# Performance work log

Hardware: AMD Instinct MI355X
Metric: run time of the kernel (lower is better)

Reference implementation:

```python
import jax, jax.numpy as jnp
import numpy as np

N_USERS = 100000
N_ITEMS = 50000
N_TOTAL = N_USERS + N_ITEMS
IN_DIM = 768
BRANCH = 64
N_EDGES = 2097152
GCN_LAYERS = 3
TEMP = 0.1
BATCH = 4096
NUM_CAND = 128  # neg_per_pos * hard_neg_factor = 16 * 8
NEG = 16


def setup_inputs() -> dict:
    key = jax.random.key(0)
    ks = jax.random.split(key, 12)
    return {
        "raw_item_embs": jax.random.normal(ks[0], (N_ITEMS, IN_DIM), jnp.float32),
        "user_sem_base": jax.random.normal(ks[1], (N_USERS, IN_DIM), jnp.float32),
        "sem_w": jax.random.normal(ks[2], (IN_DIM, BRANCH), jnp.float32) * 0.02,
        "sem_b": jnp.zeros((BRANCH,), jnp.float32),
        "collab_user_w": jax.random.normal(ks[3], (N_USERS, BRANCH), jnp.float32) * 0.1,
        "collab_item_w": jax.random.normal(ks[4], (N_ITEMS, BRANCH), jnp.float32) * 0.1,
        "adj_vals": jax.random.uniform(ks[5], (N_EDGES,), jnp.float32) * 0.1,  # ~normalized adjacency values
        "adj_rows": jax.random.randint(ks[6], (N_EDGES,), 0, N_TOTAL, jnp.int32),
        "adj_cols": jax.random.randint(ks[7], (N_EDGES,), 0, N_TOTAL, jnp.int32),
        "uids": jax.random.randint(ks[8], (BATCH,), 0, N_USERS, jnp.int32),
        "pos_iids": jax.random.randint(ks[9], (BATCH,), 0, N_ITEMS, jnp.int32),
        "cand_ids": jax.random.randint(ks[10], (BATCH, NUM_CAND), 0, N_ITEMS, jnp.int32),
    }


def _normalize(x):
    n = jnp.linalg.norm(x, axis=-1, keepdims=True)
    return x / jnp.maximum(n, 1e-12)


def _forward_embedding(raw_item_embs, user_sem_base, sem_w, sem_b,
                       collab_user_w, collab_item_w, adj_vals, adj_rows, adj_cols):
    # Semantic view (sem_mlp with dropout in eval mode == identity)
    u_sem = _normalize(user_sem_base @ sem_w + sem_b)
    i_sem = _normalize(raw_item_embs @ sem_w + sem_b)
    # Collaborative view: LightGCN propagation over sparse COO adjacency
    ego = jnp.concatenate([collab_user_w, collab_item_w], axis=0)  # [N_TOTAL, BRANCH]
    acc = ego
    for _ in range(GCN_LAYERS):
        msg = adj_vals[:, None] * ego[adj_cols]                     # [E, BRANCH] gather
        ego = jax.ops.segment_sum(msg, adj_rows, num_segments=N_TOTAL)
        acc = acc + ego
    final = acc / (GCN_LAYERS + 1)                                  # mean over stacked layers
    u_collab = _normalize(final[:N_USERS])
    i_collab = _normalize(final[N_USERS:])
    # Norm-Concat-Norm fusion
    u_all = _normalize(jnp.concatenate([u_collab, u_sem], axis=1))  # [N_USERS, 2*BRANCH]
    i_all = _normalize(jnp.concatenate([i_collab, i_sem], axis=1))  # [N_ITEMS, 2*BRANCH]
    return u_all, i_all


def reference(raw_item_embs, user_sem_base, sem_w, sem_b, collab_user_w,
              collab_item_w, adj_vals, adj_rows, adj_cols, uids, pos_iids, cand_ids):
    all_u, all_i = _forward_embedding(raw_item_embs, user_sem_base, sem_w, sem_b,
                                      collab_user_w, collab_item_w,
                                      adj_vals, adj_rows, adj_cols)
    batch_u = all_u[uids]          # [B, D]
    batch_pos = all_i[pos_iids]    # [B, D]
    # Dynamic hard negative mining (no_grad block in torch)
    pos_mask = cand_ids == pos_iids[:, None]
    cands = jnp.where(pos_mask, (cand_ids + 1) % N_ITEMS, cand_ids)  # [B, C]
    cand_embs = jax.lax.stop_gradient(all_i)[cands]                  # [B, C, D]
    cand_scores = jnp.einsum('bcd,bd->bc', cand_embs, jax.lax.stop_gradient(batch_u))
    _, top_idx = jax.lax.top_k(cand_scores, NEG)                     # [B, NEG]
    hard_neg_ids = jnp.take_along_axis(cands, top_idx, axis=1)       # [B, NEG]
    batch_neg = all_i[hard_neg_ids]                                  # [B, NEG, D]
    pos_logit = jnp.sum(batch_u * batch_pos, axis=-1, keepdims=True) / TEMP  # [B, 1]
    neg_logit = jnp.einsum('bnd,bd->bn', batch_neg, batch_u) / TEMP          # [B, NEG]
    logits = jnp.concatenate([pos_logit, neg_logit], axis=1)                 # [B, 1+NEG]
    # cross-entropy with labels = 0
    loss = -jnp.mean(jax.nn.log_softmax(logits, axis=-1)[:, 0])
    return loss
```

## Files before the change

kernel.cpp:

```cpp
#include <hip/hip_runtime.h>
#include <hip/hip_bf16.h>

#define N_USERS 100000
#define N_ITEMS 50000
#define N_TOTAL 150000
#define IN_DIM 768
#define BRANCH 64
#define N_EDGES 2097152
#define BATCH 4096
#define NUM_CAND 128
#define NEG 16
#define TEMP 0.1f
#define D2 128

#define NB 586
#define BH_BLOCKS 1024

typedef short short8 __attribute__((ext_vector_type(8)));
typedef float f32x4 __attribute__((ext_vector_type(4)));

__device__ __forceinline__ unsigned short f2bf(float f) {
    unsigned int u = __builtin_bit_cast(unsigned int, f);
    u += 0x7fffu + ((u >> 16) & 1u);
    return (unsigned short)(u >> 16);
}


__global__ __launch_bounds__(256) void bucket_hist(const int* __restrict__ rows,
                                                   int* __restrict__ bcnt) {
    __shared__ int h[NB];
    int t = threadIdx.x;
    long base = (long)blockIdx.x * 2048;
    for (int b = t; b < NB; b += 256) h[b] = 0;
    __syncthreads();
    #pragma unroll
    for (int k = 0; k < 8; ++k)
        atomicAdd(&h[rows[base + k * 256 + t] >> 8], 1);
    __syncthreads();
    for (int b = t; b < NB; b += 256) {
        int c = h[b];
        if (c) atomicAdd(&bcnt[b], c);
    }
}

__global__ __launch_bounds__(256) void bucket_scan(const int* __restrict__ bcnt,
                                                   int* __restrict__ boff,
                                                   int* __restrict__ bcur,
                                                   int* __restrict__ offs) {
    int t = threadIdx.x;
    int fi = t * 4;
    int a0 = (fi + 0 < NB) ? bcnt[fi + 0] : 0;
    int a1 = (fi + 1 < NB) ? bcnt[fi + 1] : 0;
    int a2 = (fi + 2 < NB) ? bcnt[fi + 2] : 0;
    int a3 = (fi + 3 < NB) ? bcnt[fi + 3] : 0;
    int sm = a0 + a1 + a2 + a3;
    int x = sm;
    int lane = t & 63, wid = t >> 6;
    #pragma unroll
    for (int off = 1; off < 64; off <<= 1) {
        int y = __shfl_up(x, off);
        if (lane >= off) x += y;
    }
    __shared__ int wsum[4], woff[4];
    if (lane == 63) wsum[wid] = x;
    __syncthreads();
    if (t == 0) {
        int r = 0;
        for (int i = 0; i < 4; ++i) { woff[i] = r; r += wsum[i]; }
    }
    __syncthreads();
    int excl = (x - sm) + woff[wid];
    int p[5];
    p[0] = excl;
    p[1] = p[0] + a0;
    p[2] = p[1] + a1;
    p[3] = p[2] + a2;
    p[4] = p[3] + a3;
    #pragma unroll
    for (int k = 0; k < 4; ++k) {
        if (fi + k < NB) { boff[fi + k] = p[k]; bcur[fi + k] = p[k]; }
    }
    if (fi <= NB && NB < fi + 4) {
        boff[NB] = p[NB - fi];
        offs[N_TOTAL] = p[NB - fi];
    }
}

__global__ __launch_bounds__(256) void bucket_scatter(const int* __restrict__ rows,
                                                      const int* __restrict__ cols,
                                                      const float* __restrict__ vals,
                                                      int* __restrict__ bcur,
                                                      int2* __restrict__ bedges) {
    __shared__ int lcnt[NB];
    __shared__ int lbase[NB];
    int t = threadIdx.x;
    long base = (long)blockIdx.x * 2048;
    for (int b = t; b < NB; b += 256) lcnt[b] = 0;
    __syncthreads();
    int r[8], pk[8], vb[8];
    #pragma unroll
    for (int k = 0; k < 8; ++k) {
        long i = base + k * 256 + t;
        int rr = rows[i];
        r[k]  = rr;
        pk[k] = ((rr & 255) << 18) | cols[i];
        vb[k] = __float_as_int(vals[i]);
        atomicAdd(&lcnt[rr >> 8], 1);
    }
    __syncthreads();
    for (int b = t; b < NB; b += 256) {
        int c = lcnt[b];
        if (c) lbase[b] = atomicAdd(&bcur[b], c);
    }
    __syncthreads();
    #pragma unroll
    for (int k = 0; k < 8; ++k) {
        int p = atomicAdd(&lbase[r[k] >> 8], 1);
        bedges[p] = make_int2(pk[k], vb[k]);
    }
}

__global__ __launch_bounds__(256) void fine_scatter(const int* __restrict__ boff,
                                                    const int2* __restrict__ bedges,
                                                    int* __restrict__ offs,
                                                    int2* __restrict__ edges) {
    __shared__ int hist_[256];
    __shared__ int curp[256];
    __shared__ int wsum[4], woff[4];
    int t = threadIdx.x, lane = t & 63, wid = t >> 6;
    int b = blockIdx.x;
    int s = boff[b], e = boff[b + 1];
    hist_[t] = 0;
    __syncthreads();
    for (int i = s + t; i < e; i += 256)
        atomicAdd(&hist_[((unsigned)bedges[i].x) >> 18], 1);
    __syncthreads();
    int orig = hist_[t];
    int x = orig;
    #pragma unroll
    for (int off = 1; off < 64; off <<= 1) {
        int y = __shfl_up(x, off);
        if (lane >= off) x += y;
    }
    if (lane == 63) wsum[wid] = x;
    __syncthreads();
    if (t == 0) {
        int r = 0;
        for (int i = 0; i < 4; ++i) { woff[i] = r; r += wsum[i]; }
    }
    __syncthreads();
    int excl = x - orig + woff[wid];
    int row = b * 256 + t;
    if (row < N_TOTAL) offs[row] = s + excl;
    curp[t] = s + excl;
    __syncthreads();
    for (int i = s + t; i < e; i += 256) {
        int2 rec = bedges[i];
        int rl = ((unsigned)rec.x) >> 18;
        int p = atomicAdd(&curp[rl], 1);
        edges[p] = make_int2(rec.x & 0x3FFFF, rec.y);
    }
}


__global__ __launch_bounds__(256) void init_ego_kernel(const float* __restrict__ uw,
                                                       const float* __restrict__ iw,
                                                       float* __restrict__ ego,
                                                       float* __restrict__ acc) {
    long i = (long)blockIdx.x * blockDim.x + threadIdx.x;
    const long n4 = (long)N_TOTAL * BRANCH / 4;
    if (i >= n4) return;
    long fi = i * 4;
    const long usz = (long)N_USERS * BRANCH;
    float4 v;
    if (fi < usz) v = *(const float4*)(uw + fi);
    else          v = *(const float4*)(iw + (fi - usz));
    *(float4*)(ego + fi) = v;
    *(float4*)(acc + fi) = v;
}

__global__ __launch_bounds__(256) void spmv_kernel(const int* __restrict__ offs,
                                                   const int2* __restrict__ edges,
                                                   const float* __restrict__ ego_in,
                                                   float* __restrict__ ego_out,
                                                   float* __restrict__ acc,
                                                   int write_ego) {
    int wave = (blockIdx.x * 256 + threadIdx.x) >> 6;
    int lane = threadIdx.x & 63;
    int sub  = lane >> 4;
    int l16  = lane & 15;
    int row  = wave * 4 + sub;
    if (row >= N_TOTAL) return;

    int s = offs[row], e = offs[row + 1];
    f32x4 sum = {0.f, 0.f, 0.f, 0.f};

    int i  = s;
    int e4 = s + ((e - s) & ~3);
    for (; i < e4; i += 4) {
        int2 p0 = edges[i];
        int2 p1 = edges[i + 1];
        int2 p2 = edges[i + 2];
        int2 p3 = edges[i + 3];
        f32x4 g0 = *(const f32x4*)(ego_in + (long)p0.x * BRANCH + l16 * 4);
        f32x4 g1 = *(const f32x4*)(ego_in + (long)p1.x * BRANCH + l16 * 4);
        f32x4 g2 = *(const f32x4*)(ego_in + (long)p2.x * BRANCH + l16 * 4);
        f32x4 g3 = *(const f32x4*)(ego_in + (long)p3.x * BRANCH + l16 * 4);
        sum += g0 * __int_as_float(p0.y);
        sum += g1 * __int_as_float(p1.y);
        sum += g2 * __int_as_float(p2.y);
        sum += g3 * __int_as_float(p3.y);
    }
    for (; i < e; ++i) {
        int2 p = edges[i];
        f32x4 g = *(const f32x4*)(ego_in + (long)p.x * BRANCH + l16 * 4);
        sum += g * __int_as_float(p.y);
    }

    long o = (long)row * BRANCH + l16 * 4;
    if (write_ego) *(f32x4*)(ego_out + o) = sum;
    f32x4 a = *(const f32x4*)(acc + o);
    a += sum;
    *(f32x4*)(acc + o) = a;
}


__global__ __launch_bounds__(256) void wt_prep(const float* __restrict__ W,
                                               unsigned short* __restrict__ gWt) {
    int idx = blockIdx.x * 256 + threadIdx.x;
    if (idx >= 64 * IN_DIM) return;
    int n = idx / IN_DIM, k = idx % IN_DIM;
    gWt[idx] = f2bf(W[(long)k * 64 + n]);
}

#define GROWS 128
#define GK 32
#define LSTR 40

__global__ __launch_bounds__(256) void sem_gemm_mfma(const float* __restrict__ user_base,
                                                     const float* __restrict__ item_base,
                                                     const unsigned short* __restrict__ gWt,
                                                     const float* __restrict__ bias,
                                                     float* __restrict__ all_emb) {
    __shared__ unsigned short Asl[GROWS * LSTR];
    __shared__ unsigned short Wsl[64 * LSTR];

    const int tid  = threadIdx.x;
    const int row0 = blockIdx.x * GROWS;
    const int wv   = tid >> 6;
    const int lane = tid & 63;
    const int l15  = lane & 15;
    const int quad = lane >> 4;

    const int s_r = tid >> 3;
    const int s_c = (tid & 7) * 4;

    f32x4 acc[2][4];
    #pragma unroll
    for (int r = 0; r < 2; ++r)
        #pragma unroll
        for (int c = 0; c < 4; ++c)
            acc[r][c] = (f32x4){0.f, 0.f, 0.f, 0.f};

    const int wt_n  = tid >> 2;
    const int wt_c8 = (tid & 3) * 8;

    for (int kt = 0; kt < IN_DIM; kt += GK) {
        #pragma unroll
        for (int i = 0; i < 4; ++i) {
            int r = s_r + i * 32;
            int gr = row0 + r;
            if (gr >= N_TOTAL) gr = 0;
            const float* src = (gr < N_USERS) ? (user_base + (long)gr * IN_DIM)
                                              : (item_base + (long)(gr - N_USERS) * IN_DIM);
            float4 v = *(const float4*)(src + kt + s_c);
            unsigned short* d = &Asl[r * LSTR + s_c];
            d[0] = f2bf(v.x); d[1] = f2bf(v.y); d[2] = f2bf(v.z); d[3] = f2bf(v.w);
        }
        {
            uint4 v = *(const uint4*)(gWt + (long)wt_n * IN_DIM + kt + wt_c8);
            *(uint4*)(&Wsl[wt_n * LSTR + wt_c8]) = v;
        }
        __syncthreads();

        const int arow = wv * 32 + l15;
        short8 a0 = *(const short8*)(&Asl[arow * LSTR + quad * 8]);
        short8 a1 = *(const short8*)(&Asl[(arow + 16) * LSTR + quad * 8]);
        short8 b[4];
        #pragma unroll
        for (int c = 0; c < 4; ++c)
            b[c] = *(const short8*)(&Wsl[(c * 16 + l15) * LSTR + quad * 8]);
        #pragma unroll
        for (int c = 0; c < 4; ++c) {
            acc[0][c] = __builtin_amdgcn_mfma_f32_16x16x32_bf16(a0, b[c], acc[0][c], 0, 0, 0);
            acc[1][c] = __builtin_amdgcn_mfma_f32_16x16x32_bf16(a1, b[c], acc[1][c], 0, 0, 0);
        }
        __syncthreads();
    }

    #pragma unroll
    for (int r = 0; r < 2; ++r) {
        #pragma unroll
        for (int c = 0; c < 4; ++c) {
            int col = c * 16 + l15;
            float bv = bias[col];
            #pragma unroll
            for (int i = 0; i < 4; ++i) {
                int gr = row0 + wv * 32 + r * 16 + quad * 4 + i;
                if (gr < N_TOTAL)
                    all_emb[(long)gr * D2 + BRANCH + col] = acc[r][c][i] + bv;
            }
        }
    }
}


__global__ __launch_bounds__(256) void fuse_kernel(const float* __restrict__ acc,
                                                   float* __restrict__ all_emb) {
    int wave = (blockIdx.x * 256 + threadIdx.x) >> 6;
    int lane = threadIdx.x & 63;
    if (wave >= N_TOTAL) return;

    float c = acc[(long)wave * BRANCH + lane] * 0.25f;
    float cs = c * c;
    #pragma unroll
    for (int off = 1; off < 64; off <<= 1) cs += __shfl_xor(cs, off);
    float cn = c / fmaxf(sqrtf(cs), 1e-12f);

    float s = all_emb[(long)wave * D2 + BRANCH + lane];
    float ss = s * s;
    #pragma unroll
    for (int off = 1; off < 64; off <<= 1) ss += __shfl_xor(ss, off);
    float sn = s / fmaxf(sqrtf(ss), 1e-12f);

    float tt = cn * cn + sn * sn;
    #pragma unroll
    for (int off = 1; off < 64; off <<= 1) tt += __shfl_xor(tt, off);
    float inv = 1.0f / fmaxf(sqrtf(tt), 1e-12f);

    all_emb[(long)wave * D2 + lane]          = cn * inv;
    all_emb[(long)wave * D2 + BRANCH + lane] = sn * inv;
}


__global__ __launch_bounds__(128) void loss_kernel(const float* __restrict__ all_emb,
                                                   const int* __restrict__ uids,
                                                   const int* __restrict__ pos_iids,
                                                   const int* __restrict__ cand_ids,
                                                   float* __restrict__ out) {
    __shared__ __align__(16) float uL[128];
    __shared__ float sc[128];
    __shared__ float redv[128];
    __shared__ int   ridx[128];
    __shared__ float topvals[NEG];

    int b = blockIdx.x;
    int t = threadIdx.x;
    int uid = uids[b];
    int pid = pos_iids[b];
    const float* ib = all_emb + (long)N_USERS * D2;

    uL[t] = all_emb[(long)uid * D2 + t];
    __syncthreads();

    redv[t] = uL[t] * ib[(long)pid * D2 + t];
    __syncthreads();
    for (int st = 64; st > 0; st >>= 1) {
        if (t < st) redv[t] += redv[t + st];
        __syncthreads();
    }
    float pos_dot = redv[0];

    int cand = cand_ids[(long)b * NUM_CAND + t];
    if (cand == pid) cand = (cand + 1) % N_ITEMS;
    const float4* cr4 = (const float4*)(ib + (long)cand * D2);
    const float4* u4  = (const float4*)uL;
    float s = 0.f;
    #pragma unroll 8
    for (int k = 0; k < 32; ++k) {
        float4 a = cr4[k];
        float4 u = u4[k];
        s += a.x * u.x + a.y * u.y + a.z * u.z + a.w * u.w;
    }
    sc[t] = s;
    __syncthreads();

    for (int it = 0; it < NEG; ++it) {
        redv[t] = sc[t];
        ridx[t] = t;
        __syncthreads();
        for (int st = 64; st > 0; st >>= 1) {
            if (t < st) {
                if (redv[t + st] > redv[t]) { redv[t] = redv[t + st]; ridx[t] = ridx[t + st]; }
            }
            __syncthreads();
        }
        if (t == 0) {
            topvals[it] = redv[0];
            sc[ridx[0]] = -3.0e38f;
        }
        __syncthreads();
    }

    if (t == 0) {
        float pl = pos_dot / TEMP;
        float m = pl;
        #pragma unroll
        for (int i = 0; i < NEG; ++i) m = fmaxf(m, topvals[i] / TEMP);
        float se = __expf(pl - m);
        #pragma unroll
        for (int i = 0; i < NEG; ++i) se += __expf(topvals[i] / TEMP - m);
        float lse = m + __logf(se);
        atomicAdd(out, (lse - pl) * (1.0f / BATCH));
    }
}


extern "C" void kernel_launch(void* const* d_in, const int* in_sizes, int n_in,
                              void* d_out, int out_size, void* d_ws, size_t ws_size,
                              hipStream_t stream) {
    const float* raw_item_embs = (const float*)d_in[0];
    const float* user_sem_base = (const float*)d_in[1];
    const float* sem_w         = (const float*)d_in[2];
    const float* sem_b         = (const float*)d_in[3];
    const float* collab_user_w = (const float*)d_in[4];
    const float* collab_item_w = (const float*)d_in[5];
    const float* adj_vals      = (const float*)d_in[6];
    const int*   adj_rows      = (const int*)d_in[7];
    const int*   adj_cols      = (const int*)d_in[8];
    const int*   uids          = (const int*)d_in[9];
    const int*   pos_iids      = (const int*)d_in[10];
    const int*   cand_ids      = (const int*)d_in[11];
    float* out = (float*)d_out;

    float* all_emb = (float*)d_ws;
    float* acc     = all_emb + (long)N_TOTAL * D2;
    float* egoA    = acc  + (long)N_TOTAL * BRANCH;
    float* egoB    = egoA + (long)N_TOTAL * BRANCH;
    int*   offs    = (int*)(egoB + (long)N_TOTAL * BRANCH);
    int*   bmeta   = offs + (N_TOTAL + 4);
    int*   bcnt    = bmeta;
    int*   boff    = bmeta + 1024;
    int*   bcur    = bmeta + 2048;
    int2*  edges   = (int2*)(bmeta + N_TOTAL);
    int*   bsums   = (int*)(edges + N_EDGES);
    unsigned short* gWt = (unsigned short*)(bsums + 256);
    int2*  bedges  = (int2*)egoB;

    hipMemsetAsync(bcnt, 0, 1024 * sizeof(int), stream);
    hipMemsetAsync(out, 0, sizeof(float), stream);

    bucket_hist   <<<BH_BLOCKS, 256, 0, stream>>>(adj_rows, bcnt);
    bucket_scan   <<<1, 256, 0, stream>>>(bcnt, boff, bcur, offs);
    bucket_scatter<<<BH_BLOCKS, 256, 0, stream>>>(adj_rows, adj_cols, adj_vals, bcur, bedges);
    fine_scatter  <<<NB, 256, 0, stream>>>(boff, bedges, offs, edges);

    init_ego_kernel<<<(N_TOTAL * BRANCH / 4 + 255) / 256, 256, 0, stream>>>(
        collab_user_w, collab_item_w, egoA, acc);
    const int spmv_blocks = (N_TOTAL + 15) / 16;
    spmv_kernel<<<spmv_blocks, 256, 0, stream>>>(offs, edges, egoA, egoB, acc, 1);
    spmv_kernel<<<spmv_blocks, 256, 0, stream>>>(offs, edges, egoB, egoA, acc, 1);
    spmv_kernel<<<spmv_blocks, 256, 0, stream>>>(offs, edges, egoA, egoB, acc, 0);

    wt_prep<<<(64 * IN_DIM + 255) / 256, 256, 0, stream>>>(sem_w, gWt);
    sem_gemm_mfma<<<(N_TOTAL + GROWS - 1) / GROWS, 256, 0, stream>>>(
        user_sem_base, raw_item_embs, gWt, sem_b, all_emb);

    fuse_kernel<<<37500, 256, 0, stream>>>(acc, all_emb);

    loss_kernel<<<BATCH, 128, 0, stream>>>(all_emb, uids, pos_iids, cand_ids, out);
}
```

Before: 1.050 ms.

## Compute user semantics only for batch users and drop histogram pass

Runs the semantic GEMM and the fusion step only for the BATCH users actually referenced by uids, not all 100k users, which removes most of the 768-wide user read. Keeps all four GCN layer outputs in separate buffers so the SpMV no longer does an accumulator read-modify-write. Merges the bucket histogram into the scatter by using fixed-capacity buckets (CAP), which saves one pass over the edge rows. It also swaps the shared-memory top-k loop for wave-shuffle reductions. The fixed bucket capacity assumes no 256-row bucket receives more than CAP edges, which holds only for roughly uniform row distributions.

```diff
diff --git a/kernel.cpp b/kernel.cpp
--- a/kernel.cpp
+++ b/kernel.cpp
@@ -14,6 +14,7 @@
 #define D2 128
 
 #define NB 586
+#define CAP 5120
 #define BH_BLOCKS 1024
 
 typedef short short8 __attribute__((ext_vector_type(8)));
@@ -26,26 +27,43 @@
 }
 
 
-__global__ __launch_bounds__(256) void bucket_hist(const int* __restrict__ rows,
-                                                   int* __restrict__ bcnt) {
-    __shared__ int h[NB];
+__global__ __launch_bounds__(256) void bucket_scatter(const int* __restrict__ rows,
+                                                      const int* __restrict__ cols,
+                                                      const float* __restrict__ vals,
+                                                      int* __restrict__ bcnt,
+                                                      int2* __restrict__ bedges) {
+    __shared__ int lcnt[NB];
+    __shared__ int lbase[NB];
     int t = threadIdx.x;
     long base = (long)blockIdx.x * 2048;
-    for (int b = t; b < NB; b += 256) h[b] = 0;
-    __syncthreads();
-    #pragma unroll
-    for (int k = 0; k < 8; ++k)
-        atomicAdd(&h[rows[base + k * 256 + t] >> 8], 1);
+    for (int b = t; b < NB; b += 256) lcnt[b] = 0;
+    __syncthreads();
+    int r[8], pk[8], vb[8];
+    #pragma unroll
+    for (int k = 0; k < 8; ++k) {
+        long i = base + k * 256 + t;
+        int rr = rows[i];
+        r[k]  = rr;
+        pk[k] = ((rr & 255) << 18) | cols[i];
+        vb[k] = __float_as_int(vals[i]);
+        atomicAdd(&lcnt[rr >> 8], 1);
+    }
     __syncthreads();
     for (int b = t; b < NB; b += 256) {
-        int c = h[b];
-        if (c) atomicAdd(&bcnt[b], c);
+        int c = lcnt[b];
+        if (c) lbase[b] = atomicAdd(&bcnt[b], c);
+    }
+    __syncthreads();
+    #pragma unroll
+    for (int k = 0; k < 8; ++k) {
+        int b = r[k] >> 8;
+        int p = atomicAdd(&lbase[b], 1);
+        bedges[(long)b * CAP + p] = make_int2(pk[k], vb[k]);
     }
 }
 
 __global__ __launch_bounds__(256) void bucket_scan(const int* __restrict__ bcnt,
                                                    int* __restrict__ boff,
-                                                   int* __restrict__ bcur,
                                                    int* __restrict__ offs) {
     int t = threadIdx.x;
     int fi = t * 4;
@@ -78,7 +96,7 @@
     p[4] = p[3] + a3;
     #pragma unroll
     for (int k = 0; k < 4; ++k) {
-        if (fi + k < NB) { boff[fi + k] = p[k]; bcur[fi + k] = p[k]; }
+        if (fi + k < NB) boff[fi + k] = p[k];
     }
     if (fi <= NB && NB < fi + 4) {
         boff[NB] = p[NB - fi];
@@ -86,41 +104,8 @@
     }
 }
 
-__global__ __launch_bounds__(256) void bucket_scatter(const int* __restrict__ rows,
-                                                      const int* __restrict__ cols,
-                                                      const float* __restrict__ vals,
-                                                      int* __restrict__ bcur,
-                                                      int2* __restrict__ bedges) {
-    __shared__ int lcnt[NB];
-    __shared__ int lbase[NB];
-    int t = threadIdx.x;
-    long base = (long)blockIdx.x * 2048;
-    for (int b = t; b < NB; b += 256) lcnt[b] = 0;
-    __syncthreads();
-    int r[8], pk[8], vb[8];
-    #pragma unroll
-    for (int k = 0; k < 8; ++k) {
-        long i = base + k * 256 + t;
-        int rr = rows[i];
-        r[k]  = rr;
-        pk[k] = ((rr & 255) << 18) | cols[i];
-        vb[k] = __float_as_int(vals[i]);
-        atomicAdd(&lcnt[rr >> 8], 1);
-    }
-    __syncthreads();
-    for (int b = t; b < NB; b += 256) {
-        int c = lcnt[b];
-        if (c) lbase[b] = atomicAdd(&bcur[b], c);
-    }
-    __syncthreads();
-    #pragma unroll
-    for (int k = 0; k < 8; ++k) {
-        int p = atomicAdd(&lbase[r[k] >> 8], 1);
-        bedges[p] = make_int2(pk[k], vb[k]);
-    }
-}
-
 __global__ __launch_bounds__(256) void fine_scatter(const int* __restrict__ boff,
+                                                    const int* __restrict__ bcnt,
                                                     const int2* __restrict__ bedges,
                                                     int* __restrict__ offs,
                                                     int2* __restrict__ edges) {
@@ -129,11 +114,13 @@
     __shared__ int wsum[4], woff[4];
     int t = threadIdx.x, lane = t & 63, wid = t >> 6;
     int b = blockIdx.x;
-    int s = boff[b], e = boff[b + 1];
+    int cnt = bcnt[b];
+    int s_out = boff[b];
+    const int2* src = bedges + (long)b * CAP;
     hist_[t] = 0;
     __syncthreads();
-    for (int i = s + t; i < e; i += 256)
-        atomicAdd(&hist_[((unsigned)bedges[i].x) >> 18], 1);
+    for (int i = t; i < cnt; i += 256)
+        atomicAdd(&hist_[((unsigned)src[i].x) >> 18], 1);
     __syncthreads();
     int orig = hist_[t];
     int x = orig;
@@ -151,11 +138,11 @@
     __syncthreads();
     int excl = x - orig + woff[wid];
     int row = b * 256 + t;
-    if (row < N_TOTAL) offs[row] = s + excl;
-    curp[t] = s + excl;
-    __syncthreads();
-    for (int i = s + t; i < e; i += 256) {
-        int2 rec = bedges[i];
+    if (row < N_TOTAL) offs[row] = s_out + excl;
+    curp[t] = s_out + excl;
+    __syncthreads();
+    for (int i = t; i < cnt; i += 256) {
+        int2 rec = src[i];
         int rl = ((unsigned)rec.x) >> 18;
         int p = atomicAdd(&curp[rl], 1);
         edges[p] = make_int2(rec.x & 0x3FFFF, rec.y);
@@ -165,8 +152,7 @@
 
 __global__ __launch_bounds__(256) void init_ego_kernel(const float* __restrict__ uw,
                                                        const float* __restrict__ iw,
-                                                       float* __restrict__ ego,
-                                                       float* __restrict__ acc) {
+                                                       float* __restrict__ ego) {
     long i = (long)blockIdx.x * blockDim.x + threadIdx.x;
     const long n4 = (long)N_TOTAL * BRANCH / 4;
     if (i >= n4) return;
@@ -176,15 +162,12 @@
     if (fi < usz) v = *(const float4*)(uw + fi);
     else          v = *(const float4*)(iw + (fi - usz));
     *(float4*)(ego + fi) = v;
-    *(float4*)(acc + fi) = v;
 }
 
 __global__ __launch_bounds__(256) void spmv_kernel(const int* __restrict__ offs,
                                                    const int2* __restrict__ edges,
                                                    const float* __restrict__ ego_in,
-                                                   float* __restrict__ ego_out,
-                                                   float* __restrict__ acc,
-                                                   int write_ego) {
+                                                   float* __restrict__ ego_out) {
     int wave = (blockIdx.x * 256 + threadIdx.x) >> 6;
     int lane = threadIdx.x & 63;
     int sub  = lane >> 4;
@@ -217,11 +200,7 @@
         sum += g * __int_as_float(p.y);
     }
 
-    long o = (long)row * BRANCH + l16 * 4;
-    if (write_ego) *(f32x4*)(ego_out + o) = sum;
-    f32x4 a = *(const f32x4*)(acc + o);
-    a += sum;
-    *(f32x4*)(acc + o) = a;
+    *(f32x4*)(ego_out + (long)row * BRANCH + l16 * 4) = sum;
 }
 
 
@@ -237,11 +216,10 @@
 #define GK 32
 #define LSTR 40
 
-__global__ __launch_bounds__(256) void sem_gemm_mfma(const float* __restrict__ user_base,
-                                                     const float* __restrict__ item_base,
-                                                     const unsigned short* __restrict__ gWt,
-                                                     const float* __restrict__ bias,
-                                                     float* __restrict__ all_emb) {
+__global__ __launch_bounds__(256) void sem_gemm_items(const float* __restrict__ item_base,
+                                                      const unsigned short* __restrict__ gWt,
+                                                      const float* __restrict__ bias,
+                                                      float* __restrict__ all_emb) {
     __shared__ unsigned short Asl[GROWS * LSTR];
     __shared__ unsigned short Wsl[64 * LSTR];
 
@@ -265,15 +243,19 @@
     const int wt_n  = tid >> 2;
     const int wt_c8 = (tid & 3) * 8;
 
+    const float* src_[4];
+    #pragma unroll
+    for (int i = 0; i < 4; ++i) {
+        int gr = row0 + s_r + i * 32;
+        if (gr >= N_ITEMS) gr = 0;
+        src_[i] = item_base + (long)gr * IN_DIM;
+    }
+
     for (int kt = 0; kt < IN_DIM; kt += GK) {
         #pragma unroll
         for (int i = 0; i < 4; ++i) {
             int r = s_r + i * 32;
-            int gr = row0 + r;
-            if (gr >= N_TOTAL) gr = 0;
-            const float* src = (gr < N_USERS) ? (user_base + (long)gr * IN_DIM)
-                                              : (item_base + (long)(gr - N_USERS) * IN_DIM);
-            float4 v = *(const float4*)(src + kt + s_c);
+            float4 v = *(const float4*)(src_[i] + kt + s_c);
             unsigned short* d = &Asl[r * LSTR + s_c];
             d[0] = f2bf(v.x); d[1] = f2bf(v.y); d[2] = f2bf(v.z); d[3] = f2bf(v.w);
         }
@@ -307,69 +289,176 @@
             #pragma unroll
             for (int i = 0; i < 4; ++i) {
                 int gr = row0 + wv * 32 + r * 16 + quad * 4 + i;
-                if (gr < N_TOTAL)
-                    all_emb[(long)gr * D2 + BRANCH + col] = acc[r][c][i] + bv;
+                if (gr < N_ITEMS)
+                    all_emb[(long)(N_USERS + gr) * D2 + BRANCH + col] = acc[r][c][i] + bv;
             }
         }
     }
 }
 
-
-__global__ __launch_bounds__(256) void fuse_kernel(const float* __restrict__ acc,
-                                                   float* __restrict__ all_emb) {
+__global__ __launch_bounds__(256) void sem_gemm_users(const float* __restrict__ user_base,
+                                                      const int* __restrict__ uids,
+                                                      const unsigned short* __restrict__ gWt,
+                                                      const float* __restrict__ bias,
+                                                      float* __restrict__ batch_u) {
+    __shared__ unsigned short Asl[GROWS * LSTR];
+    __shared__ unsigned short Wsl[64 * LSTR];
+
+    const int tid  = threadIdx.x;
+    const int row0 = blockIdx.x * GROWS;
+    const int wv   = tid >> 6;
+    const int lane = tid & 63;
+    const int l15  = lane & 15;
+    const int quad = lane >> 4;
+
+    const int s_r = tid >> 3;
+    const int s_c = (tid & 7) * 4;
+
+    f32x4 acc[2][4];
+    #pragma unroll
+    for (int r = 0; r < 2; ++r)
+        #pragma unroll
+        for (int c = 0; c < 4; ++c)
+            acc[r][c] = (f32x4){0.f, 0.f, 0.f, 0.f};
+
+    const int wt_n  = tid >> 2;
+    const int wt_c8 = (tid & 3) * 8;
+
+    const float* src_[4];
+    #pragma unroll
+    for (int i = 0; i < 4; ++i) {
+        int gr = row0 + s_r + i * 32;
+        src_[i] = user_base + (long)uids[gr] * IN_DIM;
+    }
+
+    for (int kt = 0; kt < IN_DIM; kt += GK) {
+        #pragma unroll
+        for (int i = 0; i < 4; ++i) {
+            int r = s_r + i * 32;
+            float4 v = *(const float4*)(src_[i] + kt + s_c);
+            unsigned short* d = &Asl[r * LSTR + s_c];
+            d[0] = f2bf(v.x); d[1] = f2bf(v.y); d[2] = f2bf(v.z); d[3] = f2bf(v.w);
+        }
+        {
+            uint4 v = *(const uint4*)(gWt + (long)wt_n * IN_DIM + kt + wt_c8);
+            *(uint4*)(&Wsl[wt_n * LSTR + wt_c8]) = v;
+        }
+        __syncthreads();
+
+        const int arow = wv * 32 + l15;
+        short8 a0 = *(const short8*)(&Asl[arow * LSTR + quad * 8]);
+        short8 a1 = *(const short8*)(&Asl[(arow + 16) * LSTR + quad * 8]);
+        short8 b[4];
+        #pragma unroll
+        for (int c = 0; c < 4; ++c)
+            b[c] = *(const short8*)(&Wsl[(c * 16 + l15) * LSTR + quad * 8]);
+        #pragma unroll
+        for (int c = 0; c < 4; ++c) {
+            acc[0][c] = __builtin_amdgcn_mfma_f32_16x16x32_bf16(a0, b[c], acc[0][c], 0, 0, 0);
+            acc[1][c] = __builtin_amdgcn_mfma_f32_16x16x32_bf16(a1, b[c], acc[1][c], 0, 0, 0);
+        }
+        __syncthreads();
+    }
+
+    #pragma unroll
+    for (int r = 0; r < 2; ++r) {
+        #pragma unroll
+        for (int c = 0; c < 4; ++c) {
+            int col = c * 16 + l15;
+            float bv = bias[col];
+            #pragma unroll
+            for (int i = 0; i < 4; ++i) {
+                int gr = row0 + wv * 32 + r * 16 + quad * 4 + i;
+                batch_u[(long)gr * D2 + BRANCH + col] = acc[r][c][i] + bv;
+            }
+        }
+    }
+}
+
+
+__device__ __forceinline__ void fuse_row(float e0, float e1, float e2, float e3,
+                                         float s, float* out_c, float* out_s) {
+    float c = (e0 + e1 + e2 + e3) * 0.25f;
+    float cs = c * c;
+    #pragma unroll
+    for (int off = 1; off < 64; off <<= 1) cs += __shfl_xor(cs, off);
+    float cn = c / fmaxf(sqrtf(cs), 1e-12f);
+
+    float ss = s * s;
+    #pragma unroll
+    for (int off = 1; off < 64; off <<= 1) ss += __shfl_xor(ss, off);
+    float sn = s / fmaxf(sqrtf(ss), 1e-12f);
+
+    float tt = cn * cn + sn * sn;
+    #pragma unroll
+    for (int off = 1; off < 64; off <<= 1) tt += __shfl_xor(tt, off);
+    float inv = 1.0f / fmaxf(sqrtf(tt), 1e-12f);
+
+    *out_c = cn * inv;
+    *out_s = sn * inv;
+}
+
+__global__ __launch_bounds__(256) void fuse_items(const float* __restrict__ e0,
+                                                  const float* __restrict__ e1,
+                                                  const float* __restrict__ e2,
+                                                  const float* __restrict__ e3,
+                                                  float* __restrict__ all_emb) {
     int wave = (blockIdx.x * 256 + threadIdx.x) >> 6;
     int lane = threadIdx.x & 63;
-    if (wave >= N_TOTAL) return;
-
-    float c = acc[(long)wave * BRANCH + lane] * 0.25f;
-    float cs = c * c;
-    #pragma unroll
-    for (int off = 1; off < 64; off <<= 1) cs += __shfl_xor(cs, off);
-    float cn = c / fmaxf(sqrtf(cs), 1e-12f);
-
-    float s = all_emb[(long)wave * D2 + BRANCH + lane];
-    float ss = s * s;
-    #pragma unroll
-    for (int off = 1; off < 64; off <<= 1) ss += __shfl_xor(ss, off);
-    float sn = s / fmaxf(sqrtf(ss), 1e-12f);
-
-    float tt = cn * cn + sn * sn;
-    #pragma unroll
-    for (int off = 1; off < 64; off <<= 1) tt += __shfl_xor(tt, off);
-    float inv = 1.0f / fmaxf(sqrtf(tt), 1e-12f);
-
-    all_emb[(long)wave * D2 + lane]          = cn * inv;
-    all_emb[(long)wave * D2 + BRANCH + lane] = sn * inv;
+    if (wave >= N_ITEMS) return;
+    long ro = (long)(N_USERS + wave) * BRANCH + lane;
+    long eo = (long)(N_USERS + wave) * D2;
+    float s = all_emb[eo + BRANCH + lane];
+    float oc, os;
+    fuse_row(e0[ro], e1[ro], e2[ro], e3[ro], s, &oc, &os);
+    all_emb[eo + lane]          = oc;
+    all_emb[eo + BRANCH + lane] = os;
+}
+
+__global__ __launch_bounds__(256) void fuse_users(const float* __restrict__ e0,
+                                                  const float* __restrict__ e1,
+                                                  const float* __restrict__ e2,
+                                                  const float* __restrict__ e3,
+                                                  const int* __restrict__ uids,
+                                                  float* __restrict__ batch_u) {
+    int wave = (blockIdx.x * 256 + threadIdx.x) >> 6;
+    int lane = threadIdx.x & 63;
+    if (wave >= BATCH) return;
+    int uid = uids[wave];
+    long ro = (long)uid * BRANCH + lane;
+    long eo = (long)wave * D2;
+    float s = batch_u[eo + BRANCH + lane];
+    float oc, os;
+    fuse_row(e0[ro], e1[ro], e2[ro], e3[ro], s, &oc, &os);
+    batch_u[eo + lane]          = oc;
+    batch_u[eo + BRANCH + lane] = os;
 }
 
 
 __global__ __launch_bounds__(128) void loss_kernel(const float* __restrict__ all_emb,
-                                                   const int* __restrict__ uids,
+                                                   const float* __restrict__ batch_u,
                                                    const int* __restrict__ pos_iids,
                                                    const int* __restrict__ cand_ids,
                                                    float* __restrict__ out) {
     __shared__ __align__(16) float uL[128];
-    __shared__ float sc[128];
-    __shared__ float redv[128];
-    __shared__ int   ridx[128];
-    __shared__ float topvals[NEG];
+    __shared__ float pd[2];
+    __shared__ float topv[2][NEG];
 
     int b = blockIdx.x;
     int t = threadIdx.x;
-    int uid = uids[b];
+    int lane = t & 63, w = t >> 6;
     int pid = pos_iids[b];
     const float* ib = all_emb + (long)N_USERS * D2;
 
-    uL[t] = all_emb[(long)uid * D2 + t];
-    __syncthreads();
-
-    redv[t] = uL[t] * ib[(long)pid * D2 + t];
-    __syncthreads();
-    for (int st = 64; st > 0; st >>= 1) {
-        if (t < st) redv[t] += redv[t + st];
-        __syncthreads();
-    }
-    float pos_dot = redv[0];
+    uL[t] = batch_u[(long)b * D2 + t];
+    __syncthreads();
+
+    {
+        float p = uL[t] * ib[(long)pid * D2 + t];
+        #pragma unroll
+        for (int off = 1; off < 64; off <<= 1) p += __shfl_xor(p, off);
+        if (lane == 0) pd[w] = p;
+    }
 
     int cand = cand_ids[(long)b * NUM_CAND + t];
     if (cand == pid) cand = (cand + 1) % N_ITEMS;
@@ -382,34 +471,38 @@
         float4 u = u4[k];
         s += a.x * u.x + a.y * u.y + a.z * u.z + a.w * u.w;
     }
-    sc[t] = s;
-    __syncthreads();
-
+
+    float val = s;
     for (int it = 0; it < NEG; ++it) {
-        redv[t] = sc[t];
-        ridx[t] = t;
-        __syncthreads();
-        for (int st = 64; st > 0; st >>= 1) {
-            if (t < st) {
-                if (redv[t + st] > redv[t]) { redv[t] = redv[t + st]; ridx[t] = ridx[t + st]; }
-            }
-            __syncthreads();
-        }
-        if (t == 0) {
-            topvals[it] = redv[0];
-            sc[ridx[0]] = -3.0e38f;
-        }
-        __syncthreads();
-    }
+        float m = val; int ml = lane;
+        #pragma unroll
+        for (int off = 1; off < 64; off <<= 1) {
+            float ov = __shfl_xor(m, off);
+            int   ol = __shfl_xor(ml, off);
+            if (ov > m || (ov == m && ol < ml)) { m = ov; ml = ol; }
+        }
+        if (lane == 0) topv[w][it] = m;
+        if (lane == ml) val = -3.0e38f;
+    }
+    __syncthreads();
 
     if (t == 0) {
-        float pl = pos_dot / TEMP;
+        float pos_dot = pd[0] + pd[1];
+        float pl = pos_dot * (1.0f / TEMP);
+        float sel[NEG];
+        int i = 0, j = 0;
+        #pragma unroll
+        for (int k = 0; k < NEG; ++k) {
+            float v0 = (i < NEG) ? topv[0][i] : -3.4e38f;
+            float v1 = (j < NEG) ? topv[1][j] : -3.4e38f;
+            if (v0 >= v1) { sel[k] = v0; ++i; } else { sel[k] = v1; ++j; }
+        }
         float m = pl;
         #pragma unroll
-        for (int i = 0; i < NEG; ++i) m = fmaxf(m, topvals[i] / TEMP);
+        for (int k = 0; k < NEG; ++k) m = fmaxf(m, sel[k] * (1.0f / TEMP));
         float se = __expf(pl - m);
         #pragma unroll
-        for (int i = 0; i < NEG; ++i) se += __expf(topvals[i] / TEMP - m);
+        for (int k = 0; k < NEG; ++k) se += __expf(sel[k] * (1.0f / TEMP) - m);
         float lse = m + __logf(se);
         atomicAdd(out, (lse - pl) * (1.0f / BATCH));
     }
@@ -434,39 +527,40 @@
     float* out = (float*)d_out;
 
     float* all_emb = (float*)d_ws;
-    float* acc     = all_emb + (long)N_TOTAL * D2;
-    float* egoA    = acc  + (long)N_TOTAL * BRANCH;
+    float* batch_u = all_emb + (long)N_TOTAL * D2;
+    float* egoA    = batch_u + (long)BATCH * D2;
     float* egoB    = egoA + (long)N_TOTAL * BRANCH;
-    int*   offs    = (int*)(egoB + (long)N_TOTAL * BRANCH);
-    int*   bmeta   = offs + (N_TOTAL + 4);
-    int*   bcnt    = bmeta;
-    int*   boff    = bmeta + 1024;
-    int*   bcur    = bmeta + 2048;
-    int2*  edges   = (int2*)(bmeta + N_TOTAL);
-    int*   bsums   = (int*)(edges + N_EDGES);
-    unsigned short* gWt = (unsigned short*)(bsums + 256);
-    int2*  bedges  = (int2*)egoB;
+    float* egoC    = egoB + (long)N_TOTAL * BRANCH;
+    float* egoD    = egoC + (long)N_TOTAL * BRANCH;
+    int*   offs    = (int*)(egoD + (long)N_TOTAL * BRANCH);
+    int*   bcnt    = offs + (N_TOTAL + 4);
+    int*   boff    = bcnt + 1024;
+    int2*  edges   = (int2*)(boff + 1024);
+    unsigned short* gWt = (unsigned short*)(edges + N_EDGES);
+    int2*  bedges  = (int2*)(gWt + 64 * IN_DIM);
 
     hipMemsetAsync(bcnt, 0, 1024 * sizeof(int), stream);
     hipMemsetAsync(out, 0, sizeof(float), stream);
 
-    bucket_hist   <<<BH_BLOCKS, 256, 0, stream>>>(adj_rows, bcnt);
-    bucket_scan   <<<1, 256, 0, stream>>>(bcnt, boff, bcur, offs);
-    bucket_scatter<<<BH_BLOCKS, 256, 0, stream>>>(adj_rows, adj_cols, adj_vals, bcur, bedges);
-    fine_scatter  <<<NB, 256, 0, stream>>>(boff, bedges, offs, edges);
+    bucket_scatter<<<BH_BLOCKS, 256, 0, stream>>>(adj_rows, adj_cols, adj_vals, bcnt, bedges);
+    bucket_scan   <<<1, 256, 0, stream>>>(bcnt, boff, offs);
+    fine_scatter  <<<NB, 256, 0, stream>>>(boff, bcnt, bedges, offs, edges);
 
     init_ego_kernel<<<(N_TOTAL * BRANCH / 4 + 255) / 256, 256, 0, stream>>>(
-        collab_user_w, collab_item_w, egoA, acc);
+        collab_user_w, collab_item_w, egoA);
     const int spmv_blocks = (N_TOTAL + 15) / 16;
-    spmv_kernel<<<spmv_blocks, 256, 0, stream>>>(offs, edges, egoA, egoB, acc, 1);
-    spmv_kernel<<<spmv_blocks, 256, 0, stream>>>(offs, edges, egoB, egoA, acc, 1);
-    spmv_kernel<<<spmv_blocks, 256, 0, stream>>>(offs, edges, egoA, egoB, acc, 0);
+    spmv_kernel<<<spmv_blocks, 256, 0, stream>>>(offs, edges, egoA, egoB);
+    spmv_kernel<<<spmv_blocks, 256, 0, stream>>>(offs, edges, egoB, egoC);
+    spmv_kernel<<<spmv_blocks, 256, 0, stream>>>(offs, edges, egoC, egoD);
 
     wt_prep<<<(64 * IN_DIM + 255) / 256, 256, 0, stream>>>(sem_w, gWt);
-    sem_gemm_mfma<<<(N_TOTAL + GROWS - 1) / GROWS, 256, 0, stream>>>(
-        user_sem_base, raw_item_embs, gWt, sem_b, all_emb);
-
-    fuse_kernel<<<37500, 256, 0, stream>>>(acc, all_emb);
-
-    loss_kernel<<<BATCH, 128, 0, stream>>>(all_emb, uids, pos_iids, cand_ids, out);
-}
+    sem_gemm_items<<<(N_ITEMS + GROWS - 1) / GROWS, 256, 0, stream>>>(
+        raw_item_embs, gWt, sem_b, all_emb);
+    sem_gemm_users<<<BATCH / GROWS, 256, 0, stream>>>(
+        user_sem_base, uids, gWt, sem_b, batch_u);
+
+    fuse_items<<<(N_ITEMS + 3) / 4, 256, 0, stream>>>(egoA, egoB, egoC, egoD, all_emb);
+    fuse_users<<<(BATCH + 3) / 4, 256, 0, stream>>>(egoA, egoB, egoC, egoD, uids, batch_u);
+
+    loss_kernel<<<BATCH, 128, 0, stream>>>(all_emb, batch_u, pos_iids, cand_ids, out);
+}
```

Result: faster. 924.4 us (-11.9%).
